# Kernel optimization log

Hardware: AMD Instinct MI355X
Metric: run time of the kernel (lower is better)

Reference implementation:

```python
import jax, jax.numpy as jnp
import numpy as np

N_NODES = 50000
N_EDGES = 640000
N_GRAPHS = 500
D = 128
N_CLASSES = 10


def setup_inputs() -> dict:
    key = jax.random.key(0)
    ks = jax.random.split(key, 12)
    x = jax.random.normal(ks[0], (N_NODES, D), dtype=jnp.float32)
    src = jax.random.randint(ks[1], (N_EDGES,), 0, N_NODES, dtype=jnp.int32)
    dst = jax.random.randint(ks[2], (N_EDGES,), 0, N_NODES, dtype=jnp.int32)
    graph_ids = jnp.sort(jax.random.randint(ks[3], (N_NODES,), 0, N_GRAPHS, dtype=jnp.int32))
    s = 1.0 / np.sqrt(D)
    W1 = jax.random.normal(ks[4], (D, D), dtype=jnp.float32) * s
    W2 = jax.random.normal(ks[5], (D, D), dtype=jnp.float32) * s
    W3 = jax.random.normal(ks[6], (D, D), dtype=jnp.float32) * s
    W4 = jax.random.normal(ks[7], (D, D), dtype=jnp.float32) * s
    Wc = jax.random.normal(ks[8], (D, N_CLASSES), dtype=jnp.float32) * s
    b1 = jnp.zeros((D,), jnp.float32)
    b2 = jnp.zeros((D,), jnp.float32)
    b3 = jnp.zeros((D,), jnp.float32)
    b4 = jnp.zeros((D,), jnp.float32)
    bc = jnp.zeros((N_CLASSES,), jnp.float32)
    return {"x": x, "src": src, "dst": dst, "graph_ids": graph_ids,
            "W1": W1, "b1": b1, "W2": W2, "b2": b2, "W3": W3, "b3": b3,
            "W4": W4, "b4": b4, "Wc": Wc, "bc": bc}


def _degree_norms(src, dst):
    ones = jnp.ones((N_EDGES,), jnp.float32)
    deg_out = jax.ops.segment_sum(ones, src, num_segments=N_NODES)
    deg_in = jax.ops.segment_sum(ones, dst, num_segments=N_NODES)
    # DGL norm='both': D_out^{-1/2} on src side, D_in^{-1/2} on dst side; inf -> 0
    norm_src = jnp.where(deg_out > 0, jax.lax.rsqrt(jnp.maximum(deg_out, 1.0)), 0.0)
    norm_dst = jnp.where(deg_in > 0, jax.lax.rsqrt(jnp.maximum(deg_in, 1.0)), 0.0)
    return norm_src, norm_dst


def _graph_conv(h, src, dst, norm_src, norm_dst, W, b):
    h = h * norm_src[:, None]
    agg = jax.ops.segment_sum(h[src], dst, num_segments=N_NODES)  # [N, D]
    agg = agg * norm_dst[:, None]
    return agg @ W + b


def reference(x, src, dst, graph_ids, W1, b1, W2, b2, W3, b3, W4, b4, Wc, bc):
    norm_src, norm_dst = _degree_norms(src, dst)
    h = jax.nn.relu(_graph_conv(x, src, dst, norm_src, norm_dst, W1, b1))
    h = jax.nn.relu(_graph_conv(h, src, dst, norm_src, norm_dst, W2, b2))
    h = jax.nn.relu(_graph_conv(h, src, dst, norm_src, norm_dst, W3, b3))
    h = jax.nn.relu(_graph_conv(h, src, dst, norm_src, norm_dst, W4, b4))
    # dgl.mean_nodes: per-graph mean of node features
    sums = jax.ops.segment_sum(h, graph_ids, num_segments=N_GRAPHS)  # [G, D]
    counts = jax.ops.segment_sum(jnp.ones((N_NODES,), jnp.float32), graph_ids, num_segments=N_GRAPHS)
    hg = sums / jnp.maximum(counts, 1.0)[:, None]
    logits = hg @ Wc + bc
    return logits, hg
```

## Files before the change

kernel.cpp:

```cpp
#include <hip/hip_runtime.h>
#include <math.h>

#define N_NODES   50000
#define N_EDGES   640000
#define N_GRAPHS  500
#define DIM       128
#define N_CLASSES 10


__global__ void zero_kernel(int* __restrict__ p, int n) {
    int i = blockIdx.x * blockDim.x + threadIdx.x;
    if (i < n) p[i] = 0;
}

__global__ void degree_kernel(const int* __restrict__ src, const int* __restrict__ dst,
                              int* __restrict__ deg_out, int* __restrict__ deg_in) {
    int i = blockIdx.x * blockDim.x + threadIdx.x;
    if (i < N_EDGES) {
        atomicAdd(&deg_out[src[i]], 1);
        atomicAdd(&deg_in[dst[i]], 1);
    }
}

__global__ void norm_kernel(const int* __restrict__ deg_out, const int* __restrict__ deg_in,
                            float* __restrict__ norm_src, float* __restrict__ norm_dst) {
    int i = blockIdx.x * blockDim.x + threadIdx.x;
    if (i < N_NODES) {
        int a = deg_out[i], b = deg_in[i];
        norm_src[i] = (a > 0) ? (1.0f / sqrtf((float)a)) : 0.0f;
        norm_dst[i] = (b > 0) ? (1.0f / sqrtf((float)b)) : 0.0f;
    }
}


__global__ void scan_phase_a(const int* __restrict__ deg, int* __restrict__ blockSums, int n) {
    __shared__ int s[256];
    int t = threadIdx.x;
    int base = blockIdx.x * 1024 + t * 4;
    int sum = 0;
#pragma unroll
    for (int i = 0; i < 4; ++i) { int idx = base + i; if (idx < n) sum += deg[idx]; }
    s[t] = sum;
    __syncthreads();
    for (int o = 128; o > 0; o >>= 1) {
        if (t < o) s[t] += s[t + o];
        __syncthreads();
    }
    if (t == 0) blockSums[blockIdx.x] = s[0];
}

__global__ void scan_sums(int* __restrict__ blockSums, int nb, int* __restrict__ row_start) {
    if (threadIdx.x == 0 && blockIdx.x == 0) {
        int acc = 0;
        for (int i = 0; i < nb; ++i) { int v = blockSums[i]; blockSums[i] = acc; acc += v; }
        row_start[N_NODES] = acc;
    }
}

__global__ void scan_phase_b(const int* __restrict__ deg, const int* __restrict__ blockSums,
                             int* __restrict__ row_start, int n) {
    __shared__ int s[256];
    int t = threadIdx.x;
    int base = blockIdx.x * 1024 + t * 4;
    int v[4]; int sum = 0;
#pragma unroll
    for (int i = 0; i < 4; ++i) { int idx = base + i; v[i] = (idx < n) ? deg[idx] : 0; sum += v[i]; }
    s[t] = sum;
    __syncthreads();
    for (int o = 1; o < 256; o <<= 1) {
        int x = (t >= o) ? s[t - o] : 0;
        __syncthreads();
        s[t] += x;
        __syncthreads();
    }
    int pre = (t > 0 ? s[t - 1] : 0) + blockSums[blockIdx.x];
#pragma unroll
    for (int i = 0; i < 4; ++i) {
        int idx = base + i;
        if (idx < n) { row_start[idx] = pre; pre += v[i]; }
    }
}

__global__ void csr_fill_kernel(const int* __restrict__ src, const int* __restrict__ dst,
                                const int* __restrict__ row_start, int* __restrict__ cursor,
                                const float* __restrict__ norm_src,
                                int* __restrict__ csr_src, float* __restrict__ csr_w) {
    int i = blockIdx.x * blockDim.x + threadIdx.x;
    if (i < N_EDGES) {
        int d = dst[i], s = src[i];
        int p = atomicAdd(&cursor[d], 1);
        int slot = row_start[d] + p;
        csr_src[slot] = s;
        csr_w[slot] = norm_src[s];
    }
}

__global__ __launch_bounds__(64) void gather_kernel(
    const float* __restrict__ h, const int* __restrict__ csr_src,
    const float* __restrict__ csr_w, const int* __restrict__ row_start,
    const float* __restrict__ norm_dst, float* __restrict__ agg)
{
    int v = blockIdx.x;
    int l = threadIdx.x;
    int p = l >> 5;
    int fq = l & 31;
    int beg = row_start[v], end = row_start[v + 1];
    __shared__ int   s_src[64];
    __shared__ float s_w[64];
    float4 acc = make_float4(0.f, 0.f, 0.f, 0.f);
    for (int base = beg; base < end; base += 64) {
        int n = min(64, end - base);
        if (l < n) { s_src[l] = csr_src[base + l]; s_w[l] = csr_w[base + l]; }
        __syncthreads();
        for (int k = p; k < n; k += 2) {
            float w = s_w[k];
            const float4 hv = *(const float4*)&h[(size_t)s_src[k] * DIM + fq * 4];
            acc.x = fmaf(w, hv.x, acc.x);
            acc.y = fmaf(w, hv.y, acc.y);
            acc.z = fmaf(w, hv.z, acc.z);
            acc.w = fmaf(w, hv.w, acc.w);
        }
        __syncthreads();
    }
    acc.x += __shfl_xor(acc.x, 32);
    acc.y += __shfl_xor(acc.y, 32);
    acc.z += __shfl_xor(acc.z, 32);
    acc.w += __shfl_xor(acc.w, 32);
    if (p == 0) {
        float nd = norm_dst[v];
        float4 o = make_float4(acc.x * nd, acc.y * nd, acc.z * nd, acc.w * nd);
        *(float4*)&agg[(size_t)v * DIM + fq * 4] = o;
    }
}

__global__ __launch_bounds__(256) void gemm_bias_relu(
    const float* __restrict__ A, const float* __restrict__ W,
    const float* __restrict__ bias, float* __restrict__ out, int nrows)
{
    __shared__ float sW[32 * 128];
    __shared__ float sA[32 * 128];
    int tid = threadIdx.x;
    int row0 = blockIdx.x * 32;
#pragma unroll
    for (int i = 0; i < 4; ++i) {
        int f4 = tid + i * 256;
        int r = f4 >> 5, c4 = f4 & 31;
        float4 v = make_float4(0.f, 0.f, 0.f, 0.f);
        if (row0 + r < nrows) v = *(const float4*)&A[(size_t)(row0 + r) * DIM + c4 * 4];
        *(float4*)&sA[r * DIM + c4 * 4] = v;
    }
    int rq = tid >> 5;
    int cc = tid & 31;
    int r0 = rq * 4, c0 = cc * 4;
    float acc[4][4];
#pragma unroll
    for (int j = 0; j < 4; ++j) {
        float bj = bias[c0 + j];
        acc[0][j] = bj; acc[1][j] = bj; acc[2][j] = bj; acc[3][j] = bj;
    }
#pragma unroll 1
    for (int kb = 0; kb < 4; ++kb) {
        __syncthreads();
#pragma unroll
        for (int i = 0; i < 4; ++i) {
            int f4 = tid + i * 256;
            int r = f4 >> 5, c4 = f4 & 31;
            *(float4*)&sW[r * DIM + c4 * 4] =
                *(const float4*)&W[(size_t)(kb * 32 + r) * DIM + c4 * 4];
        }
        __syncthreads();
#pragma unroll
        for (int k = 0; k < 32; ++k) {
            float4 w = *(float4*)&sW[k * DIM + c0];
            float a0 = sA[(r0 + 0) * DIM + kb * 32 + k];
            float a1 = sA[(r0 + 1) * DIM + kb * 32 + k];
            float a2 = sA[(r0 + 2) * DIM + kb * 32 + k];
            float a3 = sA[(r0 + 3) * DIM + kb * 32 + k];
            acc[0][0] = fmaf(a0, w.x, acc[0][0]); acc[0][1] = fmaf(a0, w.y, acc[0][1]);
            acc[0][2] = fmaf(a0, w.z, acc[0][2]); acc[0][3] = fmaf(a0, w.w, acc[0][3]);
            acc[1][0] = fmaf(a1, w.x, acc[1][0]); acc[1][1] = fmaf(a1, w.y, acc[1][1]);
            acc[1][2] = fmaf(a1, w.z, acc[1][2]); acc[1][3] = fmaf(a1, w.w, acc[1][3]);
            acc[2][0] = fmaf(a2, w.x, acc[2][0]); acc[2][1] = fmaf(a2, w.y, acc[2][1]);
            acc[2][2] = fmaf(a2, w.z, acc[2][2]); acc[2][3] = fmaf(a2, w.w, acc[2][3]);
            acc[3][0] = fmaf(a3, w.x, acc[3][0]); acc[3][1] = fmaf(a3, w.y, acc[3][1]);
            acc[3][2] = fmaf(a3, w.z, acc[3][2]); acc[3][3] = fmaf(a3, w.w, acc[3][3]);
        }
    }
#pragma unroll
    for (int i = 0; i < 4; ++i) {
        int r = row0 + r0 + i;
        if (r < nrows) {
            float4 o;
            o.x = fmaxf(acc[i][0], 0.f);
            o.y = fmaxf(acc[i][1], 0.f);
            o.z = fmaxf(acc[i][2], 0.f);
            o.w = fmaxf(acc[i][3], 0.f);
            *(float4*)&out[(size_t)r * DIM + c0] = o;
        }
    }
}

__global__ __launch_bounds__(128) void pool_kernel(
    const float* __restrict__ h, const int* __restrict__ gids,
    const float* __restrict__ Wc, const float* __restrict__ bc,
    float* __restrict__ out )
{
    int g = blockIdx.x;
    int d = threadIdx.x;
    __shared__ int s_beg, s_end;
    __shared__ float s_hg[DIM];
    if (d == 0) {
        int lo = 0, hi = N_NODES;
        while (lo < hi) { int m = (lo + hi) >> 1; if (gids[m] < g) lo = m + 1; else hi = m; }
        s_beg = lo;
        hi = N_NODES;
        while (lo < hi) { int m = (lo + hi) >> 1; if (gids[m] < g + 1) lo = m + 1; else hi = m; }
        s_end = lo;
    }
    __syncthreads();
    int beg = s_beg, end = s_end;
    float acc = 0.f;
    for (int v = beg; v < end; ++v) acc += h[(size_t)v * DIM + d];
    float cnt = (float)(end - beg);
    float hg = acc / fmaxf(cnt, 1.0f);
    out[N_GRAPHS * N_CLASSES + (size_t)g * DIM + d] = hg;
    s_hg[d] = hg;
    __syncthreads();
    if (d < N_CLASSES) {
        float a = bc[d];
        for (int k = 0; k < DIM; ++k) a = fmaf(s_hg[k], Wc[k * N_CLASSES + d], a);
        out[g * N_CLASSES + d] = a;
    }
}


extern "C" void kernel_launch(void* const* d_in, const int* in_sizes, int n_in,
                              void* d_out, int out_size, void* d_ws, size_t ws_size,
                              hipStream_t stream)
{
    const float* x   = (const float*)d_in[0];
    const int*   src = (const int*)d_in[1];
    const int*   dst = (const int*)d_in[2];
    const int*   gid = (const int*)d_in[3];
    const float* Wl[4] = { (const float*)d_in[4], (const float*)d_in[6],
                           (const float*)d_in[8], (const float*)d_in[10] };
    const float* bl[4] = { (const float*)d_in[5], (const float*)d_in[7],
                           (const float*)d_in[9], (const float*)d_in[11] };
    const float* Wc = (const float*)d_in[12];
    const float* bc = (const float*)d_in[13];
    float* out = (float*)d_out;

    char* ws = (char*)d_ws;
    size_t off = 0;
    auto alloc = [&](size_t bytes) -> char* {
        char* p = ws + off; off += (bytes + 255) & ~(size_t)255; return p;
    };
    int*   deg_out   = (int*)  alloc((size_t)N_NODES * 4);
    int*   deg_in    = (int*)  alloc((size_t)N_NODES * 4);
    int*   cursor    = (int*)  alloc((size_t)N_NODES * 4);
    float* norm_src  = (float*)alloc((size_t)N_NODES * 4);
    float* norm_dst  = (float*)alloc((size_t)N_NODES * 4);
    int*   row_start = (int*)  alloc((size_t)(N_NODES + 1) * 4);
    int*   blockSums = (int*)  alloc(64 * 4);
    int*   csr_src   = (int*)  alloc((size_t)N_EDGES * 4);
    float* csr_w     = (float*)alloc((size_t)N_EDGES * 4);
    float* bufA      = (float*)alloc((size_t)N_NODES * DIM * 4);
    float* bufB      = (float*)alloc((size_t)N_NODES * DIM * 4);
    if (off > ws_size) return;

    int zero_n = (int)(((char*)norm_src - (char*)deg_out) / 4);
    zero_kernel<<<(zero_n + 255) / 256, 256, 0, stream>>>(deg_out, zero_n);

    degree_kernel<<<(N_EDGES + 255) / 256, 256, 0, stream>>>(src, dst, deg_out, deg_in);
    norm_kernel<<<(N_NODES + 255) / 256, 256, 0, stream>>>(deg_out, deg_in, norm_src, norm_dst);

    int nb = (N_NODES + 1023) / 1024;
    scan_phase_a<<<nb, 256, 0, stream>>>(deg_in, blockSums, N_NODES);
    scan_sums<<<1, 64, 0, stream>>>(blockSums, nb, row_start);
    scan_phase_b<<<nb, 256, 0, stream>>>(deg_in, blockSums, row_start, N_NODES);

    csr_fill_kernel<<<(N_EDGES + 255) / 256, 256, 0, stream>>>(
        src, dst, row_start, cursor, norm_src, csr_src, csr_w);

    const float* h = x;
    for (int l = 0; l < 4; ++l) {
        gather_kernel<<<N_NODES, 64, 0, stream>>>(h, csr_src, csr_w, row_start, norm_dst, bufA);
        gemm_bias_relu<<<(N_NODES + 31) / 32, 256, 0, stream>>>(bufA, Wl[l], bl[l], bufB, N_NODES);
        h = bufB;
    }

    pool_kernel<<<N_GRAPHS, DIM, 0, stream>>>(bufB, gid, Wc, bc, out);
}
```

Before: 547.0 us.

## Fuse gather into GEMM layer kernel and replace degree atomics with LDS histograms

Each GCN layer now aggregates neighbour features for 32 rows directly into shared memory and then runs the dense GEMM+bias+ReLU in the same block. This removes the round trip of the aggregate buffer through global memory and halves the kernel launches per layer. Neighbour indices are broadcast with wave shuffles instead of an LDS staging loop with barriers, and two rows are loaded per iteration to raise memory-level parallelism. Degree counting moves from global atomics to per-block shared-memory histograms of packed 16-bit counters followed by a reduction pass, which reuses a feature buffer as scratch. That pass relies on no node exceeding 65535 in-edges within one block's slice.

```diff
diff --git a/kernel.cpp b/kernel.cpp
--- a/kernel.cpp
+++ b/kernel.cpp
@@ -7,29 +7,59 @@
 #define DIM       128
 #define N_CLASSES 10
 
+#define HB          64
+#define CHUNK_NODES 25000
+#define CHUNK_WORDS 12500
+
 
 __global__ void zero_kernel(int* __restrict__ p, int n) {
     int i = blockIdx.x * blockDim.x + threadIdx.x;
     if (i < n) p[i] = 0;
 }
 
-__global__ void degree_kernel(const int* __restrict__ src, const int* __restrict__ dst,
-                              int* __restrict__ deg_out, int* __restrict__ deg_in) {
-    int i = blockIdx.x * blockDim.x + threadIdx.x;
-    if (i < N_EDGES) {
-        atomicAdd(&deg_out[src[i]], 1);
-        atomicAdd(&deg_in[dst[i]], 1);
-    }
-}
-
-__global__ void norm_kernel(const int* __restrict__ deg_out, const int* __restrict__ deg_in,
-                            float* __restrict__ norm_src, float* __restrict__ norm_dst) {
-    int i = blockIdx.x * blockDim.x + threadIdx.x;
-    if (i < N_NODES) {
-        int a = deg_out[i], b = deg_in[i];
-        norm_src[i] = (a > 0) ? (1.0f / sqrtf((float)a)) : 0.0f;
-        norm_dst[i] = (b > 0) ? (1.0f / sqrtf((float)b)) : 0.0f;
-    }
+__global__ __launch_bounds__(256) void hist_kernel(
+    const int* __restrict__ src, const int* __restrict__ dst,
+    unsigned* __restrict__ partials )
+{
+    __shared__ unsigned hcnt[CHUNK_WORDS];
+    int t = threadIdx.x;
+    for (int i = t; i < CHUNK_WORDS; i += 256) hcnt[i] = 0;
+    __syncthreads();
+    const int* arr = blockIdx.z ? dst : src;
+    int lo = blockIdx.y * CHUNK_NODES;
+    int per = N_EDGES / HB;
+    int beg = blockIdx.x * per;
+    for (int i = beg + t; i < beg + per; i += 256) {
+        int v = arr[i] - lo;
+        if ((unsigned)v < (unsigned)CHUNK_NODES)
+            atomicAdd(&hcnt[v >> 1], (v & 1) ? 0x10000u : 1u);
+    }
+    __syncthreads();
+    unsigned* outp = partials +
+        (((size_t)blockIdx.z * 2 + blockIdx.y) * HB + blockIdx.x) * CHUNK_WORDS;
+    for (int i = t; i < CHUNK_WORDS; i += 256) outp[i] = hcnt[i];
+}
+
+__global__ __launch_bounds__(256) void hist_reduce(
+    const unsigned* __restrict__ partials, int* __restrict__ deg_in,
+    float* __restrict__ norm_src, float* __restrict__ norm_dst)
+{
+    int node = blockIdx.x * 256 + threadIdx.x;
+    if (node >= N_NODES) return;
+    int chunk = (node >= CHUNK_NODES) ? 1 : 0;
+    int loc = node - chunk * CHUNK_NODES;
+    int w = loc >> 1, sh = (loc & 1) << 4;
+    const unsigned* ps = partials + ((size_t)(0 * 2 + chunk) * HB) * CHUNK_WORDS + w;
+    const unsigned* pd = partials + ((size_t)(1 * 2 + chunk) * HB) * CHUNK_WORDS + w;
+    unsigned so = 0, si = 0;
+#pragma unroll 8
+    for (int b = 0; b < HB; ++b) {
+        so += (ps[(size_t)b * CHUNK_WORDS] >> sh) & 0xFFFFu;
+        si += (pd[(size_t)b * CHUNK_WORDS] >> sh) & 0xFFFFu;
+    }
+    deg_in[node] = (int)si;
+    norm_src[node] = so ? (1.0f / sqrtf((float)so)) : 0.0f;
+    norm_dst[node] = si ? (1.0f / sqrtf((float)si)) : 0.0f;
 }
 
 
@@ -95,60 +125,57 @@
     }
 }
 
-__global__ __launch_bounds__(64) void gather_kernel(
+__global__ __launch_bounds__(256) void layer_kernel(
     const float* __restrict__ h, const int* __restrict__ csr_src,
     const float* __restrict__ csr_w, const int* __restrict__ row_start,
-    const float* __restrict__ norm_dst, float* __restrict__ agg)
-{
-    int v = blockIdx.x;
-    int l = threadIdx.x;
-    int p = l >> 5;
-    int fq = l & 31;
-    int beg = row_start[v], end = row_start[v + 1];
-    __shared__ int   s_src[64];
-    __shared__ float s_w[64];
-    float4 acc = make_float4(0.f, 0.f, 0.f, 0.f);
-    for (int base = beg; base < end; base += 64) {
-        int n = min(64, end - base);
-        if (l < n) { s_src[l] = csr_src[base + l]; s_w[l] = csr_w[base + l]; }
-        __syncthreads();
-        for (int k = p; k < n; k += 2) {
-            float w = s_w[k];
-            const float4 hv = *(const float4*)&h[(size_t)s_src[k] * DIM + fq * 4];
-            acc.x = fmaf(w, hv.x, acc.x);
-            acc.y = fmaf(w, hv.y, acc.y);
-            acc.z = fmaf(w, hv.z, acc.z);
-            acc.w = fmaf(w, hv.w, acc.w);
-        }
-        __syncthreads();
-    }
-    acc.x += __shfl_xor(acc.x, 32);
-    acc.y += __shfl_xor(acc.y, 32);
-    acc.z += __shfl_xor(acc.z, 32);
-    acc.w += __shfl_xor(acc.w, 32);
-    if (p == 0) {
-        float nd = norm_dst[v];
-        float4 o = make_float4(acc.x * nd, acc.y * nd, acc.z * nd, acc.w * nd);
-        *(float4*)&agg[(size_t)v * DIM + fq * 4] = o;
-    }
-}
-
-__global__ __launch_bounds__(256) void gemm_bias_relu(
-    const float* __restrict__ A, const float* __restrict__ W,
+    const float* __restrict__ norm_dst, const float* __restrict__ W,
     const float* __restrict__ bias, float* __restrict__ out, int nrows)
 {
-    __shared__ float sW[32 * 128];
-    __shared__ float sA[32 * 128];
+    __shared__ float sA[32 * DIM];
+    __shared__ float sW[32 * DIM];
     int tid = threadIdx.x;
+    int wave = tid >> 6;
+    int lane = tid & 63;
+    int p = lane >> 5, fq = lane & 31;
     int row0 = blockIdx.x * 32;
-#pragma unroll
-    for (int i = 0; i < 4; ++i) {
-        int f4 = tid + i * 256;
-        int r = f4 >> 5, c4 = f4 & 31;
-        float4 v = make_float4(0.f, 0.f, 0.f, 0.f);
-        if (row0 + r < nrows) v = *(const float4*)&A[(size_t)(row0 + r) * DIM + c4 * 4];
-        *(float4*)&sA[r * DIM + c4 * 4] = v;
-    }
+
+    for (int r = 0; r < 8; ++r) {
+        int lrow = wave * 8 + r;
+        int v = row0 + lrow;
+        float4 acc = make_float4(0.f, 0.f, 0.f, 0.f);
+        if (v < nrows) {
+            int beg = row_start[v], end = row_start[v + 1];
+            for (int base = beg; base < end; base += 64) {
+                int n = min(64, end - base);
+                int sidx = 0; float swt = 0.f;
+                if (lane < n) { sidx = csr_src[base + lane]; swt = csr_w[base + lane]; }
+                int n4 = (n + 3) & ~3;
+                for (int k = p; k < n4; k += 4) {
+                    int i0 = __shfl(sidx, k);
+                    int i1 = __shfl(sidx, k + 2);
+                    float w0 = __shfl(swt, k);
+                    float w1 = __shfl(swt, k + 2);
+                    const float4 a = *(const float4*)&h[(size_t)i0 * DIM + fq * 4];
+                    const float4 b = *(const float4*)&h[(size_t)i1 * DIM + fq * 4];
+                    acc.x = fmaf(w0, a.x, acc.x); acc.y = fmaf(w0, a.y, acc.y);
+                    acc.z = fmaf(w0, a.z, acc.z); acc.w = fmaf(w0, a.w, acc.w);
+                    acc.x = fmaf(w1, b.x, acc.x); acc.y = fmaf(w1, b.y, acc.y);
+                    acc.z = fmaf(w1, b.z, acc.z); acc.w = fmaf(w1, b.w, acc.w);
+                }
+            }
+        }
+        acc.x += __shfl_xor(acc.x, 32);
+        acc.y += __shfl_xor(acc.y, 32);
+        acc.z += __shfl_xor(acc.z, 32);
+        acc.w += __shfl_xor(acc.w, 32);
+        if (p == 0) {
+            float nd = (v < nrows) ? norm_dst[v] : 0.0f;
+            *(float4*)&sA[lrow * DIM + fq * 4] =
+                make_float4(acc.x * nd, acc.y * nd, acc.z * nd, acc.w * nd);
+        }
+    }
+    __syncthreads();
+
     int rq = tid >> 5;
     int cc = tid & 31;
     int r0 = rq * 4, c0 = cc * 4;
@@ -255,7 +282,6 @@
     auto alloc = [&](size_t bytes) -> char* {
         char* p = ws + off; off += (bytes + 255) & ~(size_t)255; return p;
     };
-    int*   deg_out   = (int*)  alloc((size_t)N_NODES * 4);
     int*   deg_in    = (int*)  alloc((size_t)N_NODES * 4);
     int*   cursor    = (int*)  alloc((size_t)N_NODES * 4);
     float* norm_src  = (float*)alloc((size_t)N_NODES * 4);
@@ -264,15 +290,17 @@
     int*   blockSums = (int*)  alloc(64 * 4);
     int*   csr_src   = (int*)  alloc((size_t)N_EDGES * 4);
     float* csr_w     = (float*)alloc((size_t)N_EDGES * 4);
-    float* bufA      = (float*)alloc((size_t)N_NODES * DIM * 4);
-    float* bufB      = (float*)alloc((size_t)N_NODES * DIM * 4);
+    float* buf0      = (float*)alloc((size_t)N_NODES * DIM * 4);
+    float* buf1      = (float*)alloc((size_t)N_NODES * DIM * 4);
     if (off > ws_size) return;
 
-    int zero_n = (int)(((char*)norm_src - (char*)deg_out) / 4);
-    zero_kernel<<<(zero_n + 255) / 256, 256, 0, stream>>>(deg_out, zero_n);
-
-    degree_kernel<<<(N_EDGES + 255) / 256, 256, 0, stream>>>(src, dst, deg_out, deg_in);
-    norm_kernel<<<(N_NODES + 255) / 256, 256, 0, stream>>>(deg_out, deg_in, norm_src, norm_dst);
+    unsigned* partials = (unsigned*)buf1;
+
+    zero_kernel<<<(N_NODES + 255) / 256, 256, 0, stream>>>(cursor, N_NODES);
+
+    dim3 hgrid(HB, 2, 2);
+    hist_kernel<<<hgrid, 256, 0, stream>>>(src, dst, partials);
+    hist_reduce<<<(N_NODES + 255) / 256, 256, 0, stream>>>(partials, deg_in, norm_src, norm_dst);
 
     int nb = (N_NODES + 1023) / 1024;
     scan_phase_a<<<nb, 256, 0, stream>>>(deg_in, blockSums, N_NODES);
@@ -282,12 +310,11 @@
     csr_fill_kernel<<<(N_EDGES + 255) / 256, 256, 0, stream>>>(
         src, dst, row_start, cursor, norm_src, csr_src, csr_w);
 
-    const float* h = x;
-    for (int l = 0; l < 4; ++l) {
-        gather_kernel<<<N_NODES, 64, 0, stream>>>(h, csr_src, csr_w, row_start, norm_dst, bufA);
-        gemm_bias_relu<<<(N_NODES + 31) / 32, 256, 0, stream>>>(bufA, Wl[l], bl[l], bufB, N_NODES);
-        h = bufB;
-    }
-
-    pool_kernel<<<N_GRAPHS, DIM, 0, stream>>>(bufB, gid, Wc, bc, out);
-}
+    int nblk = (N_NODES + 31) / 32;
+    layer_kernel<<<nblk, 256, 0, stream>>>(x,    csr_src, csr_w, row_start, norm_dst, Wl[0], bl[0], buf0, N_NODES);
+    layer_kernel<<<nblk, 256, 0, stream>>>(buf0, csr_src, csr_w, row_start, norm_dst, Wl[1], bl[1], buf1, N_NODES);
+    layer_kernel<<<nblk, 256, 0, stream>>>(buf1, csr_src, csr_w, row_start, norm_dst, Wl[2], bl[2], buf0, N_NODES);
+    layer_kernel<<<nblk, 256, 0, stream>>>(buf0, csr_src, csr_w, row_start, norm_dst, Wl[3], bl[3], buf1, N_NODES);
+
+    pool_kernel<<<N_GRAPHS, DIM, 0, stream>>>(buf1, gid, Wc, bc, out);
+}
```

Result: faster. 492.3 us (-10.0%).
